# Kernel tuning notes

Measured on AMD Instinct MI355X. Metric: run time of the kernel, lower is better.

## Reference

```python
import jax, jax.numpy as jnp
import numpy as np

B, T, D, H = 4, 1024, 1024, 16


def setup_inputs() -> dict:
    key = jax.random.key(0)
    ks = jax.random.split(key, 6)
    s = 0.02  # small init so softmax is well-conditioned
    return {
        "x": jax.random.normal(ks[0], (B, T, D), jnp.float32),
        "position_embedding": jax.random.normal(ks[1], (B, T, D), jnp.float32),
        "Wc": jax.random.normal(ks[2], (2 * D, D), jnp.float32) * s,
        "bc": jnp.zeros((2 * D,), jnp.float32),
        "Wp": jax.random.normal(ks[3], (D, D), jnp.float32) * s,
        "bp": jnp.zeros((D,), jnp.float32),
        "Wo": jax.random.normal(ks[4], (D, D), jnp.float32) * s,
        "bo": jnp.zeros((D,), jnp.float32),
        "num_heads": H,
    }


def reference(x, position_embedding, Wc, bc, Wp, bp, Wo, bo, num_heads):
    b, t, d = x.shape
    h = num_heads
    hd = d // h
    scale = hd ** -0.5
    # content projection -> q, k  (value reuses content k, as in the original)
    cqk = (x @ Wc.T + bc).reshape(b, t, 2, h, hd)
    q = cqk[:, :, 0]  # [B,T,H,hd]
    k = cqk[:, :, 1]  # [B,T,H,hd]
    # position keys
    pk = (position_embedding @ Wp.T + bp).reshape(b, t, h, hd)
    # dual-stream scores: content-content + content-position
    scores = (jnp.einsum('bqhd,bkhd->bhqk', q, k)
              + jnp.einsum('bqhd,bkhd->bhqk', q, pk)) * scale
    attn = jax.nn.softmax(scores, axis=-1)  # dropout is identity in eval
    out = jnp.einsum('bhqk,bkhd->bqhd', attn, k).reshape(b, t, d)
    return out @ Wo.T + bo, attn
```

## Files before the change

### kernel.cpp

```cpp
#include <hip/hip_runtime.h>
#include <hip/hip_bf16.h>

#define BB 4
#define TT 1024
#define DD 1024
#define HH 16
#define HDIM 64
#define MM (BB*TT)

typedef unsigned short u16;
typedef __attribute__((ext_vector_type(8))) short bf16x8;
typedef __attribute__((ext_vector_type(8))) _Float16 f16x8;
typedef __attribute__((ext_vector_type(4))) float f32x4;
typedef __attribute__((ext_vector_type(4))) unsigned short u16x4;

__device__ __forceinline__ u16 f2bf(float f) {
    union { float f; unsigned u; } v; v.f = f;
    return (u16)((v.u + 0x7fffu + ((v.u >> 16) & 1u)) >> 16);
}
__device__ __forceinline__ float bf2f(u16 h) {
    union { unsigned u; float f; } v; v.u = ((unsigned)h) << 16; return v.f;
}
__device__ __forceinline__ u16 f2h(float f) {
    union { _Float16 h; u16 u; } v; v.h = (_Float16)f;
    return v.u;
}

__device__ __forceinline__ void gload16(const void* g, void* l) {
    __builtin_amdgcn_global_load_lds(
        (const __attribute__((address_space(1))) unsigned int*)g,
        (__attribute__((address_space(3))) unsigned int*)l, 16, 0, 0);
}

__device__ __forceinline__ void cvt_body(const float* __restrict__ src,
                                         u16* __restrict__ dst,
                                         int bid, bool to_fp16)
{
    const size_t i = ((size_t)bid * 256 + threadIdx.x) * 4;
    const float4 v = *(const float4*)&src[i];
    u16x4 o;
    if (to_fp16) { o[0] = f2h(v.x); o[1] = f2h(v.y); o[2] = f2h(v.z); o[3] = f2h(v.w); }
    else         { o[0] = f2bf(v.x); o[1] = f2bf(v.y); o[2] = f2bf(v.z); o[3] = f2bf(v.w); }
    *(u16x4*)&dst[i] = o;
}

__global__ __launch_bounds__(256)
void cvt_all_kernel(const float* __restrict__ x,  u16* __restrict__ x16,
                    const float* __restrict__ pe, u16* __restrict__ pe16,
                    const float* __restrict__ Wc, u16* __restrict__ Wc16,
                    const float* __restrict__ Wp, u16* __restrict__ Wp16,
                    const float* __restrict__ Wo, u16* __restrict__ Wo16)
{
    const int bid = blockIdx.x;
    if (bid < 4096)       cvt_body(x,  x16,  bid,        true);
    else if (bid < 8192)  cvt_body(pe, pe16, bid - 4096, true);
    else if (bid < 10240) cvt_body(Wc, Wc16, bid - 8192, true);
    else if (bid < 11264) cvt_body(Wp, Wp16, bid - 10240, true);
    else                  cvt_body(Wo, Wo16, bid - 11264, false);
}

__global__ __launch_bounds__(256)
void ktrans_kernel(const u16* __restrict__ k16, u16* __restrict__ k16T)
{
    __shared__ u16 tmp[64][72];
    const int tc = blockIdx.x, h = blockIdx.y, b = blockIdx.z;
    const size_t hb = ((size_t)(b * HH + h)) << 16;
    const int tid = threadIdx.x;
    const int sr = tid >> 2, sc = (tid & 3) * 8;
    *(bf16x8*)&tmp[sr][sc]      = *(const bf16x8*)&k16[hb + (size_t)(tc * 64 + sr) * HDIM + sc];
    *(bf16x8*)&tmp[sr][sc + 32] = *(const bf16x8*)&k16[hb + (size_t)(tc * 64 + sr) * HDIM + sc + 32];
    __syncthreads();
#pragma unroll
    for (int half = 0; half < 2; ++half) {
        bf16x8 v;
#pragma unroll
        for (int j = 0; j < 8; ++j) v[j] = (short)tmp[sc + half * 32 + j][sr];
        *(bf16x8*)&k16T[hb + (size_t)sr * TT + tc * 64 + sc + half * 32] = v;
    }
}

template<bool FP16, int MODE>
__global__ __launch_bounds__(256)
void gemm_mfma(const u16* __restrict__ Ah, const u16* __restrict__ Bh,
               const float* __restrict__ bias,
               float* __restrict__ dstF, u16* __restrict__ dstH1,
               const u16* __restrict__ kaux16,
               const int M, const int N, const int K)
{
    __shared__ u16 As[128][64];
    __shared__ u16 Bs[128][64];

    const int tid  = threadIdx.x;
    const int w    = tid >> 6;
    const int lane = tid & 63;
    const int lg   = lane >> 4;
    const int lr   = lane & 15;
    const int wr   = w >> 1, wc = w & 1;
    const int m0   = blockIdx.y * 128, n0 = blockIdx.x * 128;

    const f32x4 zero = {0.f, 0.f, 0.f, 0.f};
    f32x4 acc[4][4];
#pragma unroll
    for (int i = 0; i < 4; ++i)
#pragma unroll
        for (int j = 0; j < 4; ++j) acc[i][j] = zero;

    const int srow = tid >> 3;
    const int scol = (tid & 7) * 8;
    const int ldr  = w << 3;

    for (int k0 = 0; k0 < K; k0 += 64) {
        __syncthreads();
#pragma unroll
        for (int i = 0; i < 4; ++i) {
            const size_t ga = (size_t)(m0 + i * 32 + srow) * K + k0 + scol;
            const size_t gb = (size_t)(n0 + i * 32 + srow) * K + k0 + scol;
            gload16(&Ah[ga], &As[i * 32 + ldr][0]);
            gload16(&Bh[gb], &Bs[i * 32 + ldr][0]);
        }
        __syncthreads();
#pragma unroll
        for (int kk = 0; kk < 2; ++kk) {
            const int koff = kk * 32 + lg * 8;
#pragma unroll
            for (int mf = 0; mf < 4; ++mf) {
#pragma unroll
                for (int nf = 0; nf < 4; ++nf) {
                    if constexpr (FP16) {
                        const f16x8 a = *(const f16x8*)&As[wr * 64 + mf * 16 + lr][koff];
                        const f16x8 b = *(const f16x8*)&Bs[wc * 64 + nf * 16 + lr][koff];
                        acc[mf][nf] = __builtin_amdgcn_mfma_f32_16x16x32_f16(a, b, acc[mf][nf], 0, 0, 0);
                    } else {
                        const bf16x8 a = *(const bf16x8*)&As[wr * 64 + mf * 16 + lr][koff];
                        const bf16x8 b = *(const bf16x8*)&Bs[wc * 64 + nf * 16 + lr][koff];
                        acc[mf][nf] = __builtin_amdgcn_mfma_f32_16x16x32_bf16(a, b, acc[mf][nf], 0, 0, 0);
                    }
                }
            }
        }
    }

#pragma unroll
    for (int mf = 0; mf < 4; ++mf)
#pragma unroll
        for (int nf = 0; nf < 4; ++nf)
#pragma unroll
            for (int j = 0; j < 4; ++j) {
                const int gm = m0 + wr * 64 + mf * 16 + lg * 4 + j;
                const int gn = n0 + wc * 64 + nf * 16 + lr;
                const float v = acc[mf][nf][j] + bias[gn];
                if constexpr (MODE == 0) {
                    const int bb = gm >> 10, t = gm & 1023;
                    const int c = gn >> 10, hh = (gn & 1023) >> 6, d = gn & 63;
                    const size_t idx = ((((size_t)bb * HH + hh) << 10) + t) * HDIM + d;
                    if (c == 0) dstH1[idx] = f2bf(v * 0.125f);
                    else        ((u16*)dstF)[idx] = f2bf(v);
                } else if constexpr (MODE == 1) {
                    const int bb = gm >> 10, t = gm & 1023;
                    const int hh = gn >> 6, d = gn & 63;
                    const size_t idx = ((((size_t)bb * HH + hh) << 10) + t) * HDIM + d;
                    dstH1[idx] = f2bf(v + bf2f(kaux16[idx]));
                } else {
                    dstF[(size_t)gm * N + gn] = v;
                }
            }
}

__global__ __launch_bounds__(256)
void attn_mfma(const u16* __restrict__ qg, const u16* __restrict__ kTg,
               const u16* __restrict__ kpg,
               float* __restrict__ attn, u16* __restrict__ ch)
{
    __shared__ u16 kp_s[2][64][72];
    __shared__ u16 kT_s[2][64][72];
    __shared__ u16 P_s[4][16][72];

    const int tid  = threadIdx.x;
    const int w    = tid >> 6;
    const int lane = tid & 63;
    const int lg   = lane >> 4;
    const int lr   = lane & 15;

    const int fid = blockIdx.x;
    const int c   = fid & 7;
    const int s   = fid >> 3;
    const int g   = c + 8 * (s >> 4);
    const int q0  = (s & 15) * 64;
    const int b   = g >> 4, h = g & 15;
    const size_t hb = ((size_t)(b * HH + h)) << 16;

    bf16x8 qf0, qf1;
    {
        const size_t base = hb + (size_t)(q0 + w * 16 + lr) * HDIM + lg * 8;
        qf0 = *(const bf16x8*)&qg[base];
        qf1 = *(const bf16x8*)&qg[base + 32];
    }

    const int sr = tid >> 2;
    const int sc = (tid & 3) * 8;
    bf16x8 ra, rb, rc, rd;

    ra = *(const bf16x8*)&kpg[hb + (size_t)sr * HDIM + sc];
    rb = *(const bf16x8*)&kpg[hb + (size_t)sr * HDIM + sc + 32];
    *(bf16x8*)&kp_s[0][sr][sc]      = ra;
    *(bf16x8*)&kp_s[0][sr][sc + 32] = rb;
    __syncthreads();

    float rs[4] = {0.f, 0.f, 0.f, 0.f};
    for (int t = 0; t < TT / 64; ++t) {
        const int cur = t & 1;
        if (t < 15) {
            const size_t nb = hb + (size_t)((t + 1) * 64 + sr) * HDIM;
            ra = *(const bf16x8*)&kpg[nb + sc];
            rb = *(const bf16x8*)&kpg[nb + sc + 32];
        }
#pragma unroll
        for (int ct = 0; ct < 4; ++ct) {
            f32x4 acc = {0.f, 0.f, 0.f, 0.f};
            const bf16x8 b0 = *(const bf16x8*)&kp_s[cur][ct * 16 + lr][lg * 8];
            const bf16x8 b1 = *(const bf16x8*)&kp_s[cur][ct * 16 + lr][lg * 8 + 32];
            acc = __builtin_amdgcn_mfma_f32_16x16x32_bf16(qf0, b0, acc, 0, 0, 0);
            acc = __builtin_amdgcn_mfma_f32_16x16x32_bf16(qf1, b1, acc, 0, 0, 0);
#pragma unroll
            for (int j = 0; j < 4; ++j) rs[j] += __expf(acc[j]);
        }
        if (t < 15) {
            *(bf16x8*)&kp_s[cur ^ 1][sr][sc]      = ra;
            *(bf16x8*)&kp_s[cur ^ 1][sr][sc + 32] = rb;
        }
        __syncthreads();
    }

    ra = *(const bf16x8*)&kpg[hb + (size_t)sr * HDIM + sc];
    rb = *(const bf16x8*)&kpg[hb + (size_t)sr * HDIM + sc + 32];
    rc = *(const bf16x8*)&kTg[hb + (size_t)sr * TT + sc];
    rd = *(const bf16x8*)&kTg[hb + (size_t)sr * TT + sc + 32];
#pragma unroll
    for (int off = 1; off < 16; off <<= 1) {
#pragma unroll
        for (int j = 0; j < 4; ++j) rs[j] += __shfl_xor(rs[j], off);
    }
    float ri[4];
#pragma unroll
    for (int j = 0; j < 4; ++j) ri[j] = 1.f / rs[j];
    *(bf16x8*)&kp_s[0][sr][sc]      = ra;
    *(bf16x8*)&kp_s[0][sr][sc + 32] = rb;
    *(bf16x8*)&kT_s[0][sr][sc]      = rc;
    *(bf16x8*)&kT_s[0][sr][sc + 32] = rd;
    __syncthreads();

    f32x4 cacc[4] = {{0,0,0,0},{0,0,0,0},{0,0,0,0},{0,0,0,0}};
    const size_t abase = ((((size_t)b * HH + h) << 10) + q0 + w * 16) << 10;
    const int arow = lane >> 2;
    const int acg  = lane & 3;

    for (int t = 0; t < TT / 64; ++t) {
        const int cur = t & 1;
        if (t < 15) {
            const size_t nb = hb + (size_t)((t + 1) * 64 + sr) * HDIM;
            ra = *(const bf16x8*)&kpg[nb + sc];
            rb = *(const bf16x8*)&kpg[nb + sc + 32];
            const size_t tb = hb + (size_t)sr * TT + (t + 1) * 64;
            rc = *(const bf16x8*)&kTg[tb + sc];
            rd = *(const bf16x8*)&kTg[tb + sc + 32];
        }
#pragma unroll
        for (int ct = 0; ct < 4; ++ct) {
            f32x4 acc = {0.f, 0.f, 0.f, 0.f};
            const bf16x8 b0 = *(const bf16x8*)&kp_s[cur][ct * 16 + lr][lg * 8];
            const bf16x8 b1 = *(const bf16x8*)&kp_s[cur][ct * 16 + lr][lg * 8 + 32];
            acc = __builtin_amdgcn_mfma_f32_16x16x32_bf16(qf0, b0, acc, 0, 0, 0);
            acc = __builtin_amdgcn_mfma_f32_16x16x32_bf16(qf1, b1, acc, 0, 0, 0);
#pragma unroll
            for (int j = 0; j < 4; ++j) {
                const float p = __expf(acc[j]) * ri[j];
                P_s[w][lg * 4 + j][ct * 16 + lr] = f2bf(p);
            }
        }
        asm volatile("s_waitcnt lgkmcnt(0)" ::: "memory");
        {
            float* wbase = &attn[abase + (size_t)arow * TT + t * 64 + acg * 4];
#pragma unroll
            for (int kq = 0; kq < 4; ++kq) {
                const u16x4 pv = *(const u16x4*)&P_s[w][arow][kq * 16 + acg * 4];
                f32x4 o = {bf2f(pv[0]), bf2f(pv[1]), bf2f(pv[2]), bf2f(pv[3])};
                __builtin_nontemporal_store(o, (f32x4*)(wbase + kq * 16));
            }
        }
        const bf16x8 pa0 = *(const bf16x8*)&P_s[w][lr][lg * 8];
        const bf16x8 pa1 = *(const bf16x8*)&P_s[w][lr][lg * 8 + 32];
#pragma unroll
        for (int dt = 0; dt < 4; ++dt) {
            const bf16x8 kb0 = *(const bf16x8*)&kT_s[cur][dt * 16 + lr][lg * 8];
            const bf16x8 kb1 = *(const bf16x8*)&kT_s[cur][dt * 16 + lr][lg * 8 + 32];
            cacc[dt] = __builtin_amdgcn_mfma_f32_16x16x32_bf16(pa0, kb0, cacc[dt], 0, 0, 0);
            cacc[dt] = __builtin_amdgcn_mfma_f32_16x16x32_bf16(pa1, kb1, cacc[dt], 0, 0, 0);
        }
        if (t < 15) {
            *(bf16x8*)&kp_s[cur ^ 1][sr][sc]      = ra;
            *(bf16x8*)&kp_s[cur ^ 1][sr][sc + 32] = rb;
            *(bf16x8*)&kT_s[cur ^ 1][sr][sc]      = rc;
            *(bf16x8*)&kT_s[cur ^ 1][sr][sc + 32] = rd;
        }
        __syncthreads();
    }

#pragma unroll
    for (int dt = 0; dt < 4; ++dt)
#pragma unroll
        for (int j = 0; j < 4; ++j) {
            const int qr = q0 + w * 16 + lg * 4 + j;
            ch[(((size_t)b << 10) + qr) * DD + h * HDIM + dt * 16 + lr] = f2bf(cacc[dt][j]);
        }
}

extern "C" void kernel_launch(void* const* d_in, const int* in_sizes, int n_in,
                              void* d_out, int out_size, void* d_ws, size_t ws_size,
                              hipStream_t stream)
{
    const float* x  = (const float*)d_in[0];
    const float* pe = (const float*)d_in[1];
    const float* Wc = (const float*)d_in[2];
    const float* bc = (const float*)d_in[3];
    const float* Wp = (const float*)d_in[4];
    const float* bp = (const float*)d_in[5];
    const float* Wo = (const float*)d_in[6];
    const float* bo = (const float*)d_in[7];

    float* out  = (float*)d_out;
    float* attn = out + (size_t)MM * DD;

    char* ws = (char*)d_ws;
    u16* x16  = (u16*)(ws);
    u16* pe16 = (u16*)(ws + ((size_t)8 << 20));
    u16* Wc16 = (u16*)(ws + ((size_t)16 << 20));
    u16* Wp16 = (u16*)(ws + ((size_t)20 << 20));
    u16* Wo16 = (u16*)(ws + ((size_t)22 << 20));
    u16* q16  = (u16*)(ws + ((size_t)24 << 20));
    u16* k16  = (u16*)(ws + ((size_t)32 << 20));
    u16* kp16 = (u16*)(ws + ((size_t)40 << 20));
    u16* k16T = (u16*)(ws + ((size_t)56 << 20));
    u16* chh  = x16;

    cvt_all_kernel<<<12288, 256, 0, stream>>>(x, x16, pe, pe16, Wc, Wc16,
                                              Wp, Wp16, Wo, Wo16);
    gemm_mfma<true, 0><<<dim3(16, 32), 256, 0, stream>>>(
        x16, Wc16, bc, (float*)k16, q16, nullptr, MM, 2048, DD);
    ktrans_kernel<<<dim3(16, HH, BB), 256, 0, stream>>>(k16, k16T);
    gemm_mfma<true, 1><<<dim3(8, 32), 256, 0, stream>>>(
        pe16, Wp16, bp, nullptr, kp16, k16, MM, 1024, DD);
    attn_mfma<<<1024, 256, 0, stream>>>(q16, k16T, kp16, attn, chh);
    gemm_mfma<false, 2><<<dim3(8, 32), 256, 0, stream>>>(
        chh, Wo16, bo, out, nullptr, nullptr, MM, 1024, DD);
}
```

Before: 188.5 us.

## Cache unnormalized softmax probabilities in registers to skip score recompute pass

The attention kernel previously computed QK scores twice, once for row sums and again for normalized probabilities. It now keeps the unnormalized bf16 exp values in 128 registers per lane from the first pass and applies the reciprocal row sum at store time for attn and at the end for the PV accumulator. This removes the second score MFMA pass and the second stream of key-position loads, and lets the two LDS tiles share one buffer. The cost is much higher register pressure, which may cut occupancy or cause spills. Probabilities are now rounded to bf16 before normalization rather than after, which slightly changes numerics.

```diff
diff --git a/kernel.cpp b/kernel.cpp
--- a/kernel.cpp
+++ b/kernel.cpp
@@ -9,10 +9,12 @@
 #define MM (BB*TT)
 
 typedef unsigned short u16;
+typedef unsigned int u32;
 typedef __attribute__((ext_vector_type(8))) short bf16x8;
 typedef __attribute__((ext_vector_type(8))) _Float16 f16x8;
 typedef __attribute__((ext_vector_type(4))) float f32x4;
 typedef __attribute__((ext_vector_type(4))) unsigned short u16x4;
+typedef __attribute__((ext_vector_type(2))) unsigned int u32x2;
 
 __device__ __forceinline__ u16 f2bf(float f) {
     union { float f; unsigned u; } v; v.f = f;
@@ -171,9 +173,9 @@
                const u16* __restrict__ kpg,
                float* __restrict__ attn, u16* __restrict__ ch)
 {
-    __shared__ u16 kp_s[2][64][72];
-    __shared__ u16 kT_s[2][64][72];
+    __shared__ u16 kv_s[2][64][72];
     __shared__ u16 P_s[4][16][72];
+    __shared__ float ri_s[4][16];
 
     const int tid  = threadIdx.x;
     const int w    = tid >> 6;
@@ -198,16 +200,18 @@
 
     const int sr = tid >> 2;
     const int sc = (tid & 3) * 8;
-    bf16x8 ra, rb, rc, rd;
+    bf16x8 ra, rb;
 
     ra = *(const bf16x8*)&kpg[hb + (size_t)sr * HDIM + sc];
     rb = *(const bf16x8*)&kpg[hb + (size_t)sr * HDIM + sc + 32];
-    *(bf16x8*)&kp_s[0][sr][sc]      = ra;
-    *(bf16x8*)&kp_s[0][sr][sc + 32] = rb;
+    *(bf16x8*)&kv_s[0][sr][sc]      = ra;
+    *(bf16x8*)&kv_s[0][sr][sc + 32] = rb;
     __syncthreads();
 
-    float rs[4] = {0.f, 0.f, 0.f, 0.f};
-    for (int t = 0; t < TT / 64; ++t) {
+    u32 preg[16][8];
+    float rsum = 0.f;
+#pragma unroll
+    for (int t = 0; t < 16; ++t) {
         const int cur = t & 1;
         if (t < 15) {
             const size_t nb = hb + (size_t)((t + 1) * 64 + sr) * HDIM;
@@ -217,65 +221,55 @@
 #pragma unroll
         for (int ct = 0; ct < 4; ++ct) {
             f32x4 acc = {0.f, 0.f, 0.f, 0.f};
-            const bf16x8 b0 = *(const bf16x8*)&kp_s[cur][ct * 16 + lr][lg * 8];
-            const bf16x8 b1 = *(const bf16x8*)&kp_s[cur][ct * 16 + lr][lg * 8 + 32];
-            acc = __builtin_amdgcn_mfma_f32_16x16x32_bf16(qf0, b0, acc, 0, 0, 0);
-            acc = __builtin_amdgcn_mfma_f32_16x16x32_bf16(qf1, b1, acc, 0, 0, 0);
-#pragma unroll
-            for (int j = 0; j < 4; ++j) rs[j] += __expf(acc[j]);
+            const bf16x8 a0 = *(const bf16x8*)&kv_s[cur][ct * 16 + lr][lg * 8];
+            const bf16x8 a1 = *(const bf16x8*)&kv_s[cur][ct * 16 + lr][lg * 8 + 32];
+            acc = __builtin_amdgcn_mfma_f32_16x16x32_bf16(a0, qf0, acc, 0, 0, 0);
+            acc = __builtin_amdgcn_mfma_f32_16x16x32_bf16(a1, qf1, acc, 0, 0, 0);
+            const float p0 = __expf(acc[0]), p1 = __expf(acc[1]);
+            const float p2 = __expf(acc[2]), p3 = __expf(acc[3]);
+            rsum += (p0 + p1) + (p2 + p3);
+            preg[t][ct * 2]     = (u32)f2bf(p0) | ((u32)f2bf(p1) << 16);
+            preg[t][ct * 2 + 1] = (u32)f2bf(p2) | ((u32)f2bf(p3) << 16);
         }
         if (t < 15) {
-            *(bf16x8*)&kp_s[cur ^ 1][sr][sc]      = ra;
-            *(bf16x8*)&kp_s[cur ^ 1][sr][sc + 32] = rb;
+            *(bf16x8*)&kv_s[cur ^ 1][sr][sc]      = ra;
+            *(bf16x8*)&kv_s[cur ^ 1][sr][sc + 32] = rb;
         }
         __syncthreads();
     }
 
-    ra = *(const bf16x8*)&kpg[hb + (size_t)sr * HDIM + sc];
-    rb = *(const bf16x8*)&kpg[hb + (size_t)sr * HDIM + sc + 32];
-    rc = *(const bf16x8*)&kTg[hb + (size_t)sr * TT + sc];
-    rd = *(const bf16x8*)&kTg[hb + (size_t)sr * TT + sc + 32];
-#pragma unroll
-    for (int off = 1; off < 16; off <<= 1) {
-#pragma unroll
-        for (int j = 0; j < 4; ++j) rs[j] += __shfl_xor(rs[j], off);
-    }
-    float ri[4];
-#pragma unroll
-    for (int j = 0; j < 4; ++j) ri[j] = 1.f / rs[j];
-    *(bf16x8*)&kp_s[0][sr][sc]      = ra;
-    *(bf16x8*)&kp_s[0][sr][sc + 32] = rb;
-    *(bf16x8*)&kT_s[0][sr][sc]      = rc;
-    *(bf16x8*)&kT_s[0][sr][sc + 32] = rd;
+    ra = *(const bf16x8*)&kTg[hb + (size_t)sr * TT + sc];
+    rb = *(const bf16x8*)&kTg[hb + (size_t)sr * TT + sc + 32];
+    rsum += __shfl_xor(rsum, 16);
+    rsum += __shfl_xor(rsum, 32);
+    const float ri = 1.f / rsum;
+    if (lg == 0) ri_s[w][lr] = ri;
+    *(bf16x8*)&kv_s[0][sr][sc]      = ra;
+    *(bf16x8*)&kv_s[0][sr][sc + 32] = rb;
     __syncthreads();
+
+    const int arow = lane >> 2;
+    const int acg  = lane & 3;
+    const float ri_row = ri_s[w][arow];
+    float ri_c[4];
+#pragma unroll
+    for (int j = 0; j < 4; ++j) ri_c[j] = ri_s[w][lg * 4 + j];
 
     f32x4 cacc[4] = {{0,0,0,0},{0,0,0,0},{0,0,0,0},{0,0,0,0}};
     const size_t abase = ((((size_t)b * HH + h) << 10) + q0 + w * 16) << 10;
-    const int arow = lane >> 2;
-    const int acg  = lane & 3;
-
-    for (int t = 0; t < TT / 64; ++t) {
+
+#pragma unroll
+    for (int t = 0; t < 16; ++t) {
         const int cur = t & 1;
         if (t < 15) {
-            const size_t nb = hb + (size_t)((t + 1) * 64 + sr) * HDIM;
-            ra = *(const bf16x8*)&kpg[nb + sc];
-            rb = *(const bf16x8*)&kpg[nb + sc + 32];
             const size_t tb = hb + (size_t)sr * TT + (t + 1) * 64;
-            rc = *(const bf16x8*)&kTg[tb + sc];
-            rd = *(const bf16x8*)&kTg[tb + sc + 32];
+            ra = *(const bf16x8*)&kTg[tb + sc];
+            rb = *(const bf16x8*)&kTg[tb + sc + 32];
         }
 #pragma unroll
         for (int ct = 0; ct < 4; ++ct) {
-            f32x4 acc = {0.f, 0.f, 0.f, 0.f};
-            const bf16x8 b0 = *(const bf16x8*)&kp_s[cur][ct * 16 + lr][lg * 8];
-            const bf16x8 b1 = *(const bf16x8*)&kp_s[cur][ct * 16 + lr][lg * 8 + 32];
-            acc = __builtin_amdgcn_mfma_f32_16x16x32_bf16(qf0, b0, acc, 0, 0, 0);
-            acc = __builtin_amdgcn_mfma_f32_16x16x32_bf16(qf1, b1, acc, 0, 0, 0);
-#pragma unroll
-            for (int j = 0; j < 4; ++j) {
-                const float p = __expf(acc[j]) * ri[j];
-                P_s[w][lg * 4 + j][ct * 16 + lr] = f2bf(p);
-            }
+            u32x2 pw = {preg[t][ct * 2], preg[t][ct * 2 + 1]};
+            *(u32x2*)&P_s[w][lr][ct * 16 + lg * 4] = pw;
         }
         asm volatile("s_waitcnt lgkmcnt(0)" ::: "memory");
         {
@@ -283,7 +277,8 @@
 #pragma unroll
             for (int kq = 0; kq < 4; ++kq) {
                 const u16x4 pv = *(const u16x4*)&P_s[w][arow][kq * 16 + acg * 4];
-                f32x4 o = {bf2f(pv[0]), bf2f(pv[1]), bf2f(pv[2]), bf2f(pv[3])};
+                f32x4 o = {bf2f(pv[0]) * ri_row, bf2f(pv[1]) * ri_row,
+                           bf2f(pv[2]) * ri_row, bf2f(pv[3]) * ri_row};
                 __builtin_nontemporal_store(o, (f32x4*)(wbase + kq * 16));
             }
         }
@@ -291,16 +286,14 @@
         const bf16x8 pa1 = *(const bf16x8*)&P_s[w][lr][lg * 8 + 32];
 #pragma unroll
         for (int dt = 0; dt < 4; ++dt) {
-            const bf16x8 kb0 = *(const bf16x8*)&kT_s[cur][dt * 16 + lr][lg * 8];
-            const bf16x8 kb1 = *(const bf16x8*)&kT_s[cur][dt * 16 + lr][lg * 8 + 32];
+            const bf16x8 kb0 = *(const bf16x8*)&kv_s[cur][dt * 16 + lr][lg * 8];
+            const bf16x8 kb1 = *(const bf16x8*)&kv_s[cur][dt * 16 + lr][lg * 8 + 32];
             cacc[dt] = __builtin_amdgcn_mfma_f32_16x16x32_bf16(pa0, kb0, cacc[dt], 0, 0, 0);
             cacc[dt] = __builtin_amdgcn_mfma_f32_16x16x32_bf16(pa1, kb1, cacc[dt], 0, 0, 0);
         }
         if (t < 15) {
-            *(bf16x8*)&kp_s[cur ^ 1][sr][sc]      = ra;
-            *(bf16x8*)&kp_s[cur ^ 1][sr][sc + 32] = rb;
-            *(bf16x8*)&kT_s[cur ^ 1][sr][sc]      = rc;
-            *(bf16x8*)&kT_s[cur ^ 1][sr][sc + 32] = rd;
+            *(bf16x8*)&kv_s[cur ^ 1][sr][sc]      = ra;
+            *(bf16x8*)&kv_s[cur ^ 1][sr][sc + 32] = rb;
         }
         __syncthreads();
     }
@@ -310,7 +303,8 @@
 #pragma unroll
         for (int j = 0; j < 4; ++j) {
             const int qr = q0 + w * 16 + lg * 4 + j;
-            ch[(((size_t)b << 10) + qr) * DD + h * HDIM + dt * 16 + lr] = f2bf(cacc[dt][j]);
+            ch[(((size_t)b << 10) + qr) * DD + h * HDIM + dt * 16 + lr] =
+                f2bf(cacc[dt][j] * ri_c[j]);
         }
 }
 
```

Measured after the change: 212.0 us. 12.5% more time.
